# Performance work log

Hardware: AMD Instinct MI355X
Metric: run time of the kernel (lower is better)

Reference implementation:

```python
import jax, jax.numpy as jnp
import numpy as np

N = 50000       # nodes
E = 800000      # edges (before self-loops)
NFEAT = 256
NHID = 16       # per-head hidden dim
HEADS = 8
NCLASS = 16
NEG_SLOPE = 0.2  # PyG GATConv default leaky-relu slope


def setup_inputs() -> dict:
    key = jax.random.key(0)
    ks = jax.random.split(key, 10)
    s = 0.05  # weight scale for numerical sanity
    return {
        "x": jax.random.normal(ks[0], (N, NFEAT), jnp.float32),
        "edge_index": jax.random.randint(ks[1], (2, E), 0, N, dtype=jnp.int32),
        "W1": jax.random.normal(ks[2], (NFEAT, HEADS * NHID), jnp.float32) * s,
        "att_src1": jax.random.normal(ks[3], (HEADS, NHID), jnp.float32) * s,
        "att_dst1": jax.random.normal(ks[4], (HEADS, NHID), jnp.float32) * s,
        "b1": jnp.zeros((HEADS * NHID,), jnp.float32),
        "W2": jax.random.normal(ks[5], (HEADS * NHID, NCLASS), jnp.float32) * s,
        "att_src2": jax.random.normal(ks[6], (1, NCLASS), jnp.float32) * s,
        "att_dst2": jax.random.normal(ks[7], (1, NCLASS), jnp.float32) * s,
        "b2": jnp.zeros((NCLASS,), jnp.float32),
    }


def gat_conv(x, edge_index, W, a_src, a_dst, b, heads, out_c, concat):
    """Faithful PyG GATConv (eval mode: dropout off, add_self_loops=True)."""
    n = x.shape[0]
    loop = jnp.arange(n, dtype=edge_index.dtype)
    src = jnp.concatenate([edge_index[0], loop])  # [E+N]
    dst = jnp.concatenate([edge_index[1], loop])  # [E+N]
    h = (x @ W).reshape(n, heads, out_c)          # [N, H, C]
    # per-node attention logits
    alpha_src = jnp.einsum('nhc,hc->nh', h, a_src)  # [N, H]
    alpha_dst = jnp.einsum('nhc,hc->nh', h, a_dst)  # [N, H]
    e = jax.nn.leaky_relu(alpha_src[src] + alpha_dst[dst], NEG_SLOPE)  # [E+N, H]
    # segment softmax over incoming edges of each dst node (self-loop guarantees nonempty)
    m = jax.lax.stop_gradient(jax.ops.segment_max(e, dst, num_segments=n))
    p = jnp.exp(e - m[dst])
    denom = jax.ops.segment_sum(p, dst, num_segments=n)
    a = p / denom[dst]                              # [E+N, H]
    out = jax.ops.segment_sum(a[:, :, None] * h[src], dst, num_segments=n)  # [N, H, C]
    out = out.reshape(n, heads * out_c) if concat else out.mean(axis=1)
    return out + b


def reference(x, edge_index, W1, att_src1, att_dst1, b1, W2, att_src2, att_dst2, b2):
    h1 = jax.nn.elu(gat_conv(x, edge_index, W1, att_src1, att_dst1, b1, HEADS, NHID, True))
    return gat_conv(h1, edge_index, W2, att_src2, att_dst2, b2, 1, NCLASS, False)
```

## Files before the change

kernel.cpp:

```cpp
#include <hip/hip_runtime.h>
#include <hip/hip_bf16.h>

#define NNODES 50000
#define NEDGES 800000
#define NFEATS 256
#define NHID 16
#define HEADS 8
#define NCLS 16
#define NEG_SLOPE 0.2f
#define TOTE (NEDGES + NNODES)
#define RSTRIDE 64
#define NBUCK 196
#define NPB 256
#define BCAP 4864
#define S1_EPT 16
#define BIN_BLOCKS ((TOTE + 4095) / 4096)
#define GSTRIDE 16

typedef __attribute__((ext_vector_type(8))) short short8;
typedef __attribute__((ext_vector_type(4))) float floatx4;

static __device__ __forceinline__ short f2bf(float f) {
    __hip_bfloat16 b = __float2bfloat16(f);
    return *reinterpret_cast<short*>(&b);
}

#define AS1 __attribute__((address_space(1)))
#define AS3 __attribute__((address_space(3)))

static __device__ __forceinline__ void ld_lds16(const void* g, void* l) {
#if __has_builtin(__builtin_amdgcn_global_load_lds)
    __builtin_amdgcn_global_load_lds((const AS1 void*)g, (AS3 void*)l, 16, 0, 0);
#endif
}


__global__ __launch_bounds__(256) void k_bin(const int* __restrict__ ei,
                                             int* __restrict__ gcnt, int* __restrict__ barr,
                                             const float* __restrict__ W,
                                             const float* __restrict__ a_s,
                                             const float* __restrict__ a_d,
                                             short* __restrict__ Wsw) {
    int tid = threadIdx.x;
    if (blockIdx.x >= BIN_BLOCKS) {
        int t = (blockIdx.x - BIN_BLOCKS) * 256 + tid;
        if (t >= 4608) return;
        short8 b;
        if (t < 4096) {
            int kc = t >> 9, nt = (t >> 6) & 7, lane = t & 63;
            int quad = lane >> 4, lo = lane & 15;
#pragma unroll
            for (int j = 0; j < 8; j++)
                b[j] = f2bf(W[(size_t)(kc * 32 + quad * 8 + j) * 128 + nt * 16 + lo]);
        } else {
            int t2 = t - 4096;
            int kc = t2 >> 6, lane = t2 & 63;
            int quad = lane >> 4, lo = lane & 15;
            int h = lo & 7;
            const float* av = (lo < 8) ? (a_s + h * 16) : (a_d + h * 16);
#pragma unroll
            for (int j = 0; j < 8; j++) {
                int k = kc * 32 + quad * 8 + j;
                float acc = 0.f;
#pragma unroll
                for (int c = 0; c < 16; c++) acc += W[(size_t)k * 128 + h * 16 + c] * av[c];
                b[j] = f2bf(acc);
            }
        }
        *(short8*)(Wsw + (size_t)t * 8) = b;
        return;
    }

    __shared__ int lcnt[NBUCK], lbase[NBUCK];
    if (tid < NBUCK) lcnt[tid] = 0;
    __syncthreads();
    int e0 = blockIdx.x * (256 * S1_EPT) + tid;
    int s[S1_EPT], d[S1_EPT], rk[S1_EPT];
#pragma unroll
    for (int k = 0; k < S1_EPT; k++) {
        int e = e0 + k * 256;
        bool v = e < TOTE;
        int ss = 0, dd = 0;
        if (v) {
            if (e < NEDGES) { ss = ei[e]; dd = ei[NEDGES + e]; }
            else            { ss = e - NEDGES; dd = ss; }
        }
        s[k] = ss; d[k] = dd;
        rk[k] = v ? atomicAdd(&lcnt[dd >> 8], 1) : -1;
    }
    __syncthreads();
    if (tid < NBUCK) lbase[tid] = lcnt[tid] ? atomicAdd(&gcnt[tid * GSTRIDE], lcnt[tid]) : 0;
    __syncthreads();
#pragma unroll
    for (int k = 0; k < S1_EPT; k++) {
        if (rk[k] >= 0) {
            int b = d[k] >> 8;
            int pos = lbase[b] + rk[k];
            if (pos < BCAP)
                barr[(size_t)b * BCAP + pos] = ((d[k] & 255) << 16) | s[k];
        }
    }
}


__global__ __launch_bounds__(256) void k_csr(const int* __restrict__ gcnt,
                                             const int* __restrict__ barr,
                                             int* __restrict__ cnt, int* __restrict__ csr) {
    __shared__ int lcnt[NPB];
    __shared__ unsigned short lcsr[NPB * 65];
    int b = blockIdx.x, tid = threadIdx.x;
    lcnt[tid] = 0;
    __syncthreads();
    int n = min(gcnt[b * GSTRIDE], BCAP);
    int nodeBase = b << 8;
    for (int i = tid; i < n; i += 256) {
        int e = barr[(size_t)b * BCAP + i];
        int ln = e >> 16;
        int r = atomicAdd(&lcnt[ln], 1);
        if (r < RSTRIDE) lcsr[ln * 65 + r] = (unsigned short)(e & 0xFFFF);
    }
    __syncthreads();
    int node = nodeBase + tid;
    if (node < NNODES) cnt[node] = min(lcnt[tid], RSTRIDE);
    for (int i = tid; i < NPB * RSTRIDE; i += 256) {
        int ln = i >> 6;
        int nn = nodeBase + ln;
        if (nn < NNODES && (i & 63) < min(lcnt[ln], RSTRIDE))
            csr[(size_t)nodeBase * RSTRIDE + i] = (int)lcsr[ln * 65 + (i & 63)];
    }
}


__global__ __launch_bounds__(256) void k_gemm1(const float* __restrict__ x,
                                               const short* __restrict__ Wsw,
                                               __hip_bfloat16* __restrict__ h1,
                                               float* __restrict__ as1, float* __restrict__ ad1) {
    __shared__ short bsw[32768];
    int tid  = threadIdx.x;
    int wave = tid >> 6;
    int lane = tid & 63;
    int quad = lane >> 4;
    int lo   = lane & 15;

#if __has_builtin(__builtin_amdgcn_global_load_lds)
    {
        const char* gsrc = (const char*)Wsw + (size_t)wave * 1024 + (size_t)lane * 16;
        char* ldst = (char*)bsw + wave * 1024;
#pragma unroll
        for (int it = 0; it < 16; it++)
            ld_lds16(gsrc + it * 4096, ldst + it * 4096);
    }
#else
    {
        const uint4* g4 = (const uint4*)Wsw;
        uint4* l4 = (uint4*)bsw;
#pragma unroll
        for (int it = 0; it < 16; it++) l4[it * 256 + tid] = g4[it * 256 + tid];
    }
#endif
    short8 wafr[8];
#pragma unroll
    for (int kc = 0; kc < 8; kc++)
        wafr[kc] = *(const short8*)(Wsw + (size_t)(4096 + kc * 64 + lane) * 8);
    __syncthreads();

    int rowBase = blockIdx.x * 128 + wave * 32;
    const float* xa[2];
#pragma unroll
    for (int mt = 0; mt < 2; mt++) {
        int row = rowBase + mt * 16 + lo;
        row = (row < NNODES) ? row : (NNODES - 1);
        xa[mt] = x + (size_t)row * 256 + quad * 8;
    }

    floatx4 acc[2][8], accA[2];
#pragma unroll
    for (int mt = 0; mt < 2; mt++) {
        accA[mt] = (floatx4){0.f, 0.f, 0.f, 0.f};
#pragma unroll
        for (int nt = 0; nt < 8; nt++) acc[mt][nt] = (floatx4){0.f, 0.f, 0.f, 0.f};
    }

    float4 a0[2], a1[2];
#pragma unroll
    for (int mt = 0; mt < 2; mt++) {
        a0[mt] = *(const float4*)(xa[mt]);
        a1[mt] = *(const float4*)(xa[mt] + 4);
    }

    for (int kc = 0; kc < 8; kc++) {
        float4 n0[2], n1[2];
        if (kc < 7) {
#pragma unroll
            for (int mt = 0; mt < 2; mt++) {
                n0[mt] = *(const float4*)(xa[mt] + (kc + 1) * 32);
                n1[mt] = *(const float4*)(xa[mt] + (kc + 1) * 32 + 4);
            }
        }
        short8 afr[2];
#pragma unroll
        for (int mt = 0; mt < 2; mt++) {
            union { short8 s; __hip_bfloat162 h[4]; } u;
            u.h[0] = __float22bfloat162_rn(make_float2(a0[mt].x, a0[mt].y));
            u.h[1] = __float22bfloat162_rn(make_float2(a0[mt].z, a0[mt].w));
            u.h[2] = __float22bfloat162_rn(make_float2(a1[mt].x, a1[mt].y));
            u.h[3] = __float22bfloat162_rn(make_float2(a1[mt].z, a1[mt].w));
            afr[mt] = u.s;
        }
#pragma unroll
        for (int nt = 0; nt < 8; nt++) {
            short8 bfr = *(const short8*)&bsw[((kc * 8 + nt) * 64 + lane) * 8];
            acc[0][nt] = __builtin_amdgcn_mfma_f32_16x16x32_bf16(afr[0], bfr, acc[0][nt], 0, 0, 0);
            acc[1][nt] = __builtin_amdgcn_mfma_f32_16x16x32_bf16(afr[1], bfr, acc[1][nt], 0, 0, 0);
        }
        accA[0] = __builtin_amdgcn_mfma_f32_16x16x32_bf16(afr[0], wafr[kc], accA[0], 0, 0, 0);
        accA[1] = __builtin_amdgcn_mfma_f32_16x16x32_bf16(afr[1], wafr[kc], accA[1], 0, 0, 0);
#pragma unroll
        for (int mt = 0; mt < 2; mt++) { a0[mt] = n0[mt]; a1[mt] = n1[mt]; }
    }

#pragma unroll
    for (int mt = 0; mt < 2; mt++)
#pragma unroll
        for (int nt = 0; nt < 8; nt++)
#pragma unroll
            for (int reg = 0; reg < 4; reg++) {
                int row = rowBase + mt * 16 + quad * 4 + reg;
                int col = nt * 16 + lo;
                if (row < NNODES)
                    h1[(size_t)row * 128 + col] = __float2bfloat16(acc[mt][nt][reg]);
            }
#pragma unroll
    for (int mt = 0; mt < 2; mt++)
#pragma unroll
        for (int reg = 0; reg < 4; reg++) {
            int row = rowBase + mt * 16 + quad * 4 + reg;
            if (row < NNODES) {
                float v = accA[mt][reg];
                if (lo < 8) as1[(size_t)row * 8 + lo] = v;
                else        ad1[(size_t)row * 8 + (lo - 8)] = v;
            }
        }
}


__global__ __launch_bounds__(256) void k_agg1(const int* __restrict__ cnt, const int* __restrict__ csr,
                                              const __hip_bfloat16* __restrict__ h1,
                                              const float* __restrict__ as1, const float* __restrict__ ad1,
                                              const float* __restrict__ b1, __hip_bfloat16* __restrict__ h1act) {
    int node = blockIdx.x * 4 + (threadIdx.x >> 6);
    int lane = threadIdx.x & 63;
    int cl   = lane & 15;
    int slot = lane >> 4;
    int head = cl >> 1;
    int deg  = min(cnt[node], RSTRIDE);
    float adst = ad1[node * 8 + head];
    int rowv = csr[node * RSTRIDE + lane];

    float acc[8] = {0.f, 0.f, 0.f, 0.f, 0.f, 0.f, 0.f, 0.f};
    float s = 0.f;
    for (int i2 = 0; i2 < deg; i2 += 8) {
        int ia = i2 + slot;
        int ib = ia + 4;
        int sa = __shfl(rowv, ia & 63);
        int sb = __shfl(rowv, ib & 63);
        union { short8 v; __hip_bfloat162 h[4]; } ua, ub;
        float pa = 0.f, pb = 0.f;
        ua.v = (short8){0, 0, 0, 0, 0, 0, 0, 0};
        ub.v = (short8){0, 0, 0, 0, 0, 0, 0, 0};
        if (ia < deg) {
            ua.v = *(const short8*)(h1 + (size_t)sa * 128 + cl * 8);
            float e = as1[sa * 8 + head] + adst;
            e = (e > 0.f) ? e : NEG_SLOPE * e;
            pa = __expf(e);
        }
        if (ib < deg) {
            ub.v = *(const short8*)(h1 + (size_t)sb * 128 + cl * 8);
            float e = as1[sb * 8 + head] + adst;
            e = (e > 0.f) ? e : NEG_SLOPE * e;
            pb = __expf(e);
        }
        s += pa + pb;
#pragma unroll
        for (int q = 0; q < 4; q++) {
            float2 fa = __bfloat1622float2(ua.h[q]);
            float2 fb = __bfloat1622float2(ub.h[q]);
            acc[q * 2]     = fmaf(pa, fa.x, acc[q * 2]);
            acc[q * 2 + 1] = fmaf(pa, fa.y, acc[q * 2 + 1]);
            acc[q * 2]     = fmaf(pb, fb.x, acc[q * 2]);
            acc[q * 2 + 1] = fmaf(pb, fb.y, acc[q * 2 + 1]);
        }
    }
#pragma unroll
    for (int q = 0; q < 8; q++) {
        acc[q] += __shfl_xor(acc[q], 16);
        acc[q] += __shfl_xor(acc[q], 32);
    }
    s += __shfl_xor(s, 16);
    s += __shfl_xor(s, 32);
    if (slot == 0) {
        float is = 1.f / s;
        union { short8 v; short us[8]; } pk;
#pragma unroll
        for (int q = 0; q < 8; q++) {
            float v = acc[q] * is + b1[cl * 8 + q];
            v = (v > 0.f) ? v : (__expf(v) - 1.f);
            pk.us[q] = f2bf(v);
        }
        *(short8*)(h1act + (size_t)node * 128 + cl * 8) = pk.v;
    }
}


__global__ __launch_bounds__(256) void k_gemm2(const __hip_bfloat16* __restrict__ h1act,
                                               const float* __restrict__ W2,
                                               const float* __restrict__ a_src,
                                               const float* __restrict__ a_dst,
                                               float* __restrict__ h2,
                                               float* __restrict__ as2, float* __restrict__ ad2) {
    __shared__ float w[128 * 16];
    __shared__ float hr[16][129];
    int tid = threadIdx.x;
    int row0 = blockIdx.x * 16;
    for (int i = tid; i < 2048; i += 256) w[i] = W2[i];
    {
        int r = tid >> 4, k8 = (tid & 15) * 8;
        int gr = row0 + r;
        union { short8 v; __hip_bfloat162 h[4]; } u;
        if (gr < NNODES) u.v = *(const short8*)(h1act + (size_t)gr * 128 + k8);
        else             u.v = (short8){0, 0, 0, 0, 0, 0, 0, 0};
#pragma unroll
        for (int q = 0; q < 4; q++) {
            float2 f = __bfloat1622float2(u.h[q]);
            hr[r][k8 + q * 2]     = f.x;
            hr[r][k8 + q * 2 + 1] = f.y;
        }
    }
    __syncthreads();
    int r = tid >> 4, c = tid & 15;
    float acc = 0.f;
#pragma unroll 8
    for (int k = 0; k < 128; k++) acc += hr[r][k] * w[k * 16 + c];
    int gr = row0 + r;
    if (gr < NNODES) h2[(size_t)gr * 16 + c] = acc;
    float sv = acc * a_src[c];
    float dv = acc * a_dst[c];
#pragma unroll
    for (int o = 1; o <= 8; o <<= 1) {
        sv += __shfl_xor(sv, o);
        dv += __shfl_xor(dv, o);
    }
    if (c == 0 && gr < NNODES) { as2[gr] = sv; ad2[gr] = dv; }
}


__global__ __launch_bounds__(256) void k_agg2(const int* __restrict__ cnt, const int* __restrict__ csr,
                                              const float* __restrict__ h2, const float* __restrict__ as2,
                                              const float* __restrict__ ad2, const float* __restrict__ b2,
                                              float* __restrict__ out) {
    int node = blockIdx.x * 4 + (threadIdx.x >> 6);
    int lane = threadIdx.x & 63;
    int c4   = lane & 3;
    int slot = lane >> 2;
    int deg  = min(cnt[node], RSTRIDE);
    float adst = ad2[node];
    int rowv = csr[node * RSTRIDE + lane];

    float4 acc = make_float4(0.f, 0.f, 0.f, 0.f);
    float s = 0.f;
    for (int i2 = 0; i2 < deg; i2 += 16) {
        int ia = i2 + slot;
        int sa = __shfl(rowv, ia & 63);
        float p0 = 0.f;
        float4 r0 = make_float4(0.f, 0.f, 0.f, 0.f);
        if (ia < deg) {
            r0 = *(const float4*)(h2 + (size_t)sa * 16 + c4 * 4);
            float e = as2[sa] + adst;
            e = (e > 0.f) ? e : NEG_SLOPE * e;
            p0 = __expf(e);
        }
        s += p0;
        acc.x = fmaf(p0, r0.x, acc.x);
        acc.y = fmaf(p0, r0.y, acc.y);
        acc.z = fmaf(p0, r0.z, acc.z);
        acc.w = fmaf(p0, r0.w, acc.w);
    }
#pragma unroll
    for (int o = 4; o <= 32; o <<= 1) {
        acc.x += __shfl_xor(acc.x, o);
        acc.y += __shfl_xor(acc.y, o);
        acc.z += __shfl_xor(acc.z, o);
        acc.w += __shfl_xor(acc.w, o);
        s += __shfl_xor(s, o);
    }
    if (slot == 0) {
        float is = 1.f / s;
        float4 o4;
        o4.x = acc.x * is + b2[c4 * 4 + 0];
        o4.y = acc.y * is + b2[c4 * 4 + 1];
        o4.z = acc.z * is + b2[c4 * 4 + 2];
        o4.w = acc.w * is + b2[c4 * 4 + 3];
        *(float4*)(out + (size_t)node * 16 + c4 * 4) = o4;
    }
}


extern "C" void kernel_launch(void* const* d_in, const int* in_sizes, int n_in,
                              void* d_out, int out_size, void* d_ws, size_t ws_size,
                              hipStream_t stream) {
    const float* x    = (const float*)d_in[0];
    const int*   ei   = (const int*)d_in[1];
    const float* W1   = (const float*)d_in[2];
    const float* a_s1 = (const float*)d_in[3];
    const float* a_d1 = (const float*)d_in[4];
    const float* b1   = (const float*)d_in[5];
    const float* W2   = (const float*)d_in[6];
    const float* a_s2 = (const float*)d_in[7];
    const float* a_d2 = (const float*)d_in[8];
    const float* b2   = (const float*)d_in[9];
    float* out = (float*)d_out;

    char* p = (char*)d_ws;
    auto alloc = [&](size_t bytes) -> char* {
        char* q = p;
        p += (bytes + 255) & ~(size_t)255;
        return q;
    };
    int*  gcnt = (int*)alloc((size_t)NBUCK * GSTRIDE * 4);
    int*  barr = (int*)alloc((size_t)NBUCK * BCAP * 4);
    int*  cnt  = (int*)alloc((size_t)NNODES * 4);
    int*  csr  = (int*)alloc((size_t)NNODES * RSTRIDE * 4);
    short* Wsw = (short*)alloc((size_t)36864 * 2);
    __hip_bfloat16* h1 = (__hip_bfloat16*)alloc((size_t)NNODES * 128 * 2);
    float* as1 = (float*)alloc((size_t)NNODES * 8 * 4);
    float* ad1 = (float*)alloc((size_t)NNODES * 8 * 4);
    __hip_bfloat16* h1act = (__hip_bfloat16*)alloc((size_t)NNODES * 128 * 2);
    float* h2  = (float*)as1;
    float* as2 = (float*)barr;
    float* ad2 = (float*)barr + NNODES;

    hipMemsetAsync(gcnt, 0, (size_t)NBUCK * GSTRIDE * 4, stream);
    hipLaunchKernelGGL(k_bin,   dim3(BIN_BLOCKS + 18), dim3(256), 0, stream,
                       ei, gcnt, barr, W1, a_s1, a_d1, Wsw);
    hipLaunchKernelGGL(k_csr,   dim3(NBUCK), dim3(256), 0, stream, gcnt, barr, cnt, csr);
    hipLaunchKernelGGL(k_gemm1, dim3((NNODES + 127) / 128), dim3(256), 0, stream, x, Wsw, h1, as1, ad1);
    hipLaunchKernelGGL(k_agg1,  dim3(NNODES / 4), dim3(256), 0, stream, cnt, csr, h1, as1, ad1, b1, h1act);
    hipLaunchKernelGGL(k_gemm2, dim3((NNODES + 15) / 16), dim3(256), 0, stream, h1act, W2, a_s2, a_d2, h2, as2, ad2);
    hipLaunchKernelGGL(k_agg2,  dim3(NNODES / 4), dim3(256), 0, stream, cnt, csr, h2, as2, ad2, b2, out);
}
```

Before: 221.4 us.

## Merge CSR build with GEMM1 into one launch and widen aggregation loads

```diff
diff --git a/kernel.cpp b/kernel.cpp
--- a/kernel.cpp
+++ b/kernel.cpp
@@ -16,6 +16,7 @@
 #define S1_EPT 16
 #define BIN_BLOCKS ((TOTE + 4095) / 4096)
 #define GSTRIDE 16
+#define GEMM1_BLOCKS ((NNODES + 127) / 128)
 
 typedef __attribute__((ext_vector_type(8))) short short8;
 typedef __attribute__((ext_vector_type(4))) float floatx4;
@@ -103,40 +104,44 @@
 }
 
 
-__global__ __launch_bounds__(256) void k_csr(const int* __restrict__ gcnt,
+__global__ __launch_bounds__(256) void k_mid(const int* __restrict__ gcnt,
                                              const int* __restrict__ barr,
-                                             int* __restrict__ cnt, int* __restrict__ csr) {
-    __shared__ int lcnt[NPB];
-    __shared__ unsigned short lcsr[NPB * 65];
-    int b = blockIdx.x, tid = threadIdx.x;
-    lcnt[tid] = 0;
-    __syncthreads();
-    int n = min(gcnt[b * GSTRIDE], BCAP);
-    int nodeBase = b << 8;
-    for (int i = tid; i < n; i += 256) {
-        int e = barr[(size_t)b * BCAP + i];
-        int ln = e >> 16;
-        int r = atomicAdd(&lcnt[ln], 1);
-        if (r < RSTRIDE) lcsr[ln * 65 + r] = (unsigned short)(e & 0xFFFF);
-    }
-    __syncthreads();
-    int node = nodeBase + tid;
-    if (node < NNODES) cnt[node] = min(lcnt[tid], RSTRIDE);
-    for (int i = tid; i < NPB * RSTRIDE; i += 256) {
-        int ln = i >> 6;
-        int nn = nodeBase + ln;
-        if (nn < NNODES && (i & 63) < min(lcnt[ln], RSTRIDE))
-            csr[(size_t)nodeBase * RSTRIDE + i] = (int)lcsr[ln * 65 + (i & 63)];
-    }
-}
-
-
-__global__ __launch_bounds__(256) void k_gemm1(const float* __restrict__ x,
-                                               const short* __restrict__ Wsw,
-                                               __hip_bfloat16* __restrict__ h1,
-                                               float* __restrict__ as1, float* __restrict__ ad1) {
-    __shared__ short bsw[32768];
-    int tid  = threadIdx.x;
+                                             int* __restrict__ cnt, int* __restrict__ csr,
+                                             const float* __restrict__ x,
+                                             const short* __restrict__ Wsw,
+                                             __hip_bfloat16* __restrict__ h1,
+                                             float* __restrict__ as1, float* __restrict__ ad1) {
+    __shared__ short smem[32768];
+    int tid = threadIdx.x;
+
+    if (blockIdx.x < NBUCK) {
+        int* lcnt = (int*)smem;
+        unsigned short* lcsr = (unsigned short*)smem + 512;
+        int b = blockIdx.x;
+        lcnt[tid] = 0;
+        __syncthreads();
+        int n = min(gcnt[b * GSTRIDE], BCAP);
+        int nodeBase = b << 8;
+        for (int i = tid; i < n; i += 256) {
+            int e = barr[(size_t)b * BCAP + i];
+            int ln = e >> 16;
+            int r = atomicAdd(&lcnt[ln], 1);
+            if (r < RSTRIDE) lcsr[ln * 65 + r] = (unsigned short)(e & 0xFFFF);
+        }
+        __syncthreads();
+        int node = nodeBase + tid;
+        if (node < NNODES) cnt[node] = min(lcnt[tid], RSTRIDE);
+        for (int i = tid; i < NPB * RSTRIDE; i += 256) {
+            int ln = i >> 6;
+            int nn = nodeBase + ln;
+            if (nn < NNODES && (i & 63) < min(lcnt[ln], RSTRIDE))
+                csr[(size_t)nodeBase * RSTRIDE + i] = (int)lcsr[ln * 65 + (i & 63)];
+        }
+        return;
+    }
+
+    short* bsw = smem;
+    int bid  = blockIdx.x - NBUCK;
     int wave = tid >> 6;
     int lane = tid & 63;
     int quad = lane >> 4;
@@ -164,7 +169,7 @@
         wafr[kc] = *(const short8*)(Wsw + (size_t)(4096 + kc * 64 + lane) * 8);
     __syncthreads();
 
-    int rowBase = blockIdx.x * 128 + wave * 32;
+    int rowBase = bid * 128 + wave * 32;
     const float* xa[2];
 #pragma unroll
     for (int mt = 0; mt < 2; mt++) {
@@ -259,37 +264,31 @@
 
     float acc[8] = {0.f, 0.f, 0.f, 0.f, 0.f, 0.f, 0.f, 0.f};
     float s = 0.f;
-    for (int i2 = 0; i2 < deg; i2 += 8) {
-        int ia = i2 + slot;
-        int ib = ia + 4;
-        int sa = __shfl(rowv, ia & 63);
-        int sb = __shfl(rowv, ib & 63);
-        union { short8 v; __hip_bfloat162 h[4]; } ua, ub;
-        float pa = 0.f, pb = 0.f;
-        ua.v = (short8){0, 0, 0, 0, 0, 0, 0, 0};
-        ub.v = (short8){0, 0, 0, 0, 0, 0, 0, 0};
-        if (ia < deg) {
-            ua.v = *(const short8*)(h1 + (size_t)sa * 128 + cl * 8);
-            float e = as1[sa * 8 + head] + adst;
-            e = (e > 0.f) ? e : NEG_SLOPE * e;
-            pa = __expf(e);
-        }
-        if (ib < deg) {
-            ub.v = *(const short8*)(h1 + (size_t)sb * 128 + cl * 8);
-            float e = as1[sb * 8 + head] + adst;
-            e = (e > 0.f) ? e : NEG_SLOPE * e;
-            pb = __expf(e);
-        }
-        s += pa + pb;
-#pragma unroll
-        for (int q = 0; q < 4; q++) {
-            float2 fa = __bfloat1622float2(ua.h[q]);
-            float2 fb = __bfloat1622float2(ub.h[q]);
-            acc[q * 2]     = fmaf(pa, fa.x, acc[q * 2]);
-            acc[q * 2 + 1] = fmaf(pa, fa.y, acc[q * 2 + 1]);
-            acc[q * 2]     = fmaf(pb, fb.x, acc[q * 2]);
-            acc[q * 2 + 1] = fmaf(pb, fb.y, acc[q * 2 + 1]);
-        }
+    for (int i2 = 0; i2 < deg; i2 += 16) {
+        float p[4];
+        union { short8 v; __hip_bfloat162 h[4]; } u[4];
+#pragma unroll
+        for (int t = 0; t < 4; t++) {
+            int ii = i2 + slot + t * 4;
+            int src = __shfl(rowv, ii & 63);
+            p[t] = 0.f;
+            u[t].v = (short8){0, 0, 0, 0, 0, 0, 0, 0};
+            if (ii < deg) {
+                u[t].v = *(const short8*)(h1 + (size_t)src * 128 + cl * 8);
+                float e = as1[src * 8 + head] + adst;
+                e = (e > 0.f) ? e : NEG_SLOPE * e;
+                p[t] = __expf(e);
+            }
+        }
+        s += (p[0] + p[1]) + (p[2] + p[3]);
+#pragma unroll
+        for (int t = 0; t < 4; t++)
+#pragma unroll
+            for (int q = 0; q < 4; q++) {
+                float2 f = __bfloat1622float2(u[t].h[q]);
+                acc[q * 2]     = fmaf(p[t], f.x, acc[q * 2]);
+                acc[q * 2 + 1] = fmaf(p[t], f.y, acc[q * 2 + 1]);
+            }
     }
 #pragma unroll
     for (int q = 0; q < 8; q++) {
@@ -368,22 +367,31 @@
 
     float4 acc = make_float4(0.f, 0.f, 0.f, 0.f);
     float s = 0.f;
-    for (int i2 = 0; i2 < deg; i2 += 16) {
+    for (int i2 = 0; i2 < deg; i2 += 32) {
         int ia = i2 + slot;
+        int ib = ia + 16;
         int sa = __shfl(rowv, ia & 63);
-        float p0 = 0.f;
+        int sb = __shfl(rowv, ib & 63);
+        float p0 = 0.f, p1 = 0.f;
         float4 r0 = make_float4(0.f, 0.f, 0.f, 0.f);
+        float4 r1 = make_float4(0.f, 0.f, 0.f, 0.f);
         if (ia < deg) {
             r0 = *(const float4*)(h2 + (size_t)sa * 16 + c4 * 4);
             float e = as2[sa] + adst;
             e = (e > 0.f) ? e : NEG_SLOPE * e;
             p0 = __expf(e);
         }
-        s += p0;
-        acc.x = fmaf(p0, r0.x, acc.x);
-        acc.y = fmaf(p0, r0.y, acc.y);
-        acc.z = fmaf(p0, r0.z, acc.z);
-        acc.w = fmaf(p0, r0.w, acc.w);
+        if (ib < deg) {
+            r1 = *(const float4*)(h2 + (size_t)sb * 16 + c4 * 4);
+            float e = as2[sb] + adst;
+            e = (e > 0.f) ? e : NEG_SLOPE * e;
+            p1 = __expf(e);
+        }
+        s += p0 + p1;
+        acc.x = fmaf(p0, r0.x, fmaf(p1, r1.x, acc.x));
+        acc.y = fmaf(p0, r0.y, fmaf(p1, r1.y, acc.y));
+        acc.z = fmaf(p0, r0.z, fmaf(p1, r1.z, acc.z));
+        acc.w = fmaf(p0, r0.w, fmaf(p1, r1.w, acc.w));
     }
 #pragma unroll
     for (int o = 4; o <= 32; o <<= 1) {
@@ -442,8 +450,8 @@
     hipMemsetAsync(gcnt, 0, (size_t)NBUCK * GSTRIDE * 4, stream);
     hipLaunchKernelGGL(k_bin,   dim3(BIN_BLOCKS + 18), dim3(256), 0, stream,
                        ei, gcnt, barr, W1, a_s1, a_d1, Wsw);
-    hipLaunchKernelGGL(k_csr,   dim3(NBUCK), dim3(256), 0, stream, gcnt, barr, cnt, csr);
-    hipLaunchKernelGGL(k_gemm1, dim3((NNODES + 127) / 128), dim3(256), 0, stream, x, Wsw, h1, as1, ad1);
+    hipLaunchKernelGGL(k_mid,   dim3(NBUCK + GEMM1_BLOCKS), dim3(256), 0, stream,
+                       gcnt, barr, cnt, csr, x, Wsw, h1, as1, ad1);
     hipLaunchKernelGGL(k_agg1,  dim3(NNODES / 4), dim3(256), 0, stream, cnt, csr, h1, as1, ad1, b1, h1act);
     hipLaunchKernelGGL(k_gemm2, dim3((NNODES + 15) / 16), dim3(256), 0, stream, h1act, W2, a_s2, a_d2, h2, as2, ad2);
     hipLaunchKernelGGL(k_agg2,  dim3(NNODES / 4), dim3(256), 0, stream, cnt, csr, h2, as2, ad2, b2, out);
```

New measurement: 209.1 us. 5.5% less time.
